# Performance work log

Measured on AMD Instinct MI355X. Metric: run time of the kernel, lower is better.

## Reference

```python
import jax, jax.numpy as jnp
import numpy as np

N, E = 100000, 1600000
D_IN, H, C = 128, 4, 32
NEG_SLOPE = 0.2

def setup_inputs() -> dict:
    key = jax.random.key(0)
    ks = jax.random.split(key, 6)
    x = jax.random.normal(ks[0], (N, D_IN), dtype=jnp.float32)
    edge_index = jax.random.randint(ks[1], (2, E), 0, N, dtype=jnp.int64)
    s = 1.0 / np.sqrt(D_IN)
    W_l = jax.random.normal(ks[2], (D_IN, H * C), dtype=jnp.float32) * s
    W_r = jax.random.normal(ks[3], (D_IN, H * C), dtype=jnp.float32) * s
    att = jax.random.normal(ks[4], (H, C), dtype=jnp.float32) * (1.0 / np.sqrt(C))
    bias = jax.random.normal(ks[5], (H * C,), dtype=jnp.float32) * 0.01
    return {"x": x, "edge_index": edge_index, "W_l": W_l, "W_r": W_r, "att": att, "bias": bias}

def reference(x, edge_index, W_l, W_r, att, bias):
    # GATv2: e_ij = att . LeakyReLU(W_l x_j + W_r x_i); softmax over incoming edges of i;
    # out_i = sum_j alpha_ij * (W_l x_j); heads concatenated, then bias.
    src, dst = edge_index[0], edge_index[1]
    n = x.shape[0]
    xl = (x @ W_l).reshape(n, H, C)   # source transform (lin_l)
    xr = (x @ W_r).reshape(n, H, C)   # target transform (lin_r)
    xj = xl[src]                       # [E,H,C] gathered source feats
    xi = xr[dst]                       # [E,H,C] gathered target feats
    e = jax.nn.leaky_relu(xi + xj, NEG_SLOPE)
    score = jnp.einsum('ehc,hc->eh', e, att)          # [E,H]
    # segment softmax over destination nodes
    m = jax.ops.segment_max(score, dst, num_segments=n)  # [N,H]
    ex = jnp.exp(score - m[dst])
    denom = jax.ops.segment_sum(ex, dst, num_segments=n)  # [N,H]
    alpha = ex / (denom[dst] + 1e-16)                      # [E,H]
    out = jax.ops.segment_sum(alpha[..., None] * xj, dst, num_segments=n)  # [N,H,C]
    return out.reshape(n, H * C) + bias
```

## Files before the change

### kernel.cpp

```cpp
#include <hip/hip_runtime.h>
#include <hip/hip_bf16.h>
#include <math.h>

#define N_NODES 100000
#define E_EDGES 1600000
#define D 128
#define NEG_SLOPE 0.2f

#define BSH   8
#define NBKT  391
#define BCAP  4992
#define P1_EPB 8192
#define P1_TPB 512
#define P1_EPT 16

typedef __bf16 bf16x8 __attribute__((ext_vector_type(8)));
typedef float f32x4 __attribute__((ext_vector_type(4)));
typedef float f32x2 __attribute__((ext_vector_type(2)));

__device__ __forceinline__ float bf2f(unsigned short u) {
    union { unsigned int i; float f; } x; x.i = ((unsigned int)u) << 16; return x.f;
}
__device__ __forceinline__ unsigned short f2bf(float f) {
    union { float f; unsigned int i; } x; x.f = f;
    unsigned int r = x.i + 0x7fffu + ((x.i >> 16) & 1u);
    return (unsigned short)(r >> 16);
}
__device__ __forceinline__ void unpack4p(uint2 u, f32x2* lo, f32x2* hi) {
    union { unsigned int i; float f; } a, b, c, d;
    a.i = u.x << 16; b.i = u.x & 0xffff0000u;
    c.i = u.y << 16; d.i = u.y & 0xffff0000u;
    *lo = (f32x2){a.f, b.f}; *hi = (f32x2){c.f, d.f};
}
__device__ __forceinline__ f32x2 pabs(f32x2 v) {
    union { f32x2 f; unsigned int u[2]; } x; x.f = v;
    x.u[0] &= 0x7fffffffu; x.u[1] &= 0x7fffffffu;
    return x.f;
}

__global__ void GATv2Conv_56908316672629_kernel(
    const unsigned int* ei_words, int* flags,
    const float* __restrict__ Wl, const float* __restrict__ Wr,
    unsigned short* __restrict__ wtg, int* __restrict__ bcur)
{
    __shared__ int cnt_edge;
    const int tid = threadIdx.x;
    const int bid = blockIdx.x;

    if (bid == 0) {
        for (int i = tid; i < NBKT; i += 256) bcur[i] = 0;
    }
    if (bid == 1) {
        if (tid == 0) cnt_edge = 0;
        __syncthreads();
        unsigned int w = ei_words[2 * tid + 1];
        if (w != 0u) atomicAdd(&cnt_edge, 1);
        __syncthreads();
        if (tid == 0) flags[0] = (cnt_edge == 0) ? 1 : 0;
    }

    const int gid = bid * 256 + tid;
    const int sel = gid >> 14;
    const int rem = gid & 16383;
    const int k = rem >> 7, n = rem & 127;
    const float* W = sel ? Wr : Wl;
    wtg[(size_t)sel * 16384 + n * 128 + k] = f2bf(W[k * 128 + n]);
}

__global__ __launch_bounds__(256) void gemm_f32_kernel(
    const float* __restrict__ X,
    const unsigned short* __restrict__ wtg,
    unsigned short* __restrict__ xl, unsigned short* __restrict__ xr)
{
    __shared__ unsigned short Xs[128][136];

    const int rowbase = blockIdx.x * 128;
    const int tid = threadIdx.x;

    for (int c = tid; c < 4096; c += 256) {
        int r = c >> 5, k4 = (c & 31) << 2;
        int grow = rowbase + r;
        float4 v = make_float4(0.f, 0.f, 0.f, 0.f);
        if (grow < N_NODES) v = ((const float4*)(X + (size_t)grow * D))[c & 31];
        union { unsigned short us[4]; uint2 u2; } pk;
        pk.us[0] = f2bf(v.x); pk.us[1] = f2bf(v.y);
        pk.us[2] = f2bf(v.z); pk.us[3] = f2bf(v.w);
        *((uint2*)&Xs[r][k4]) = pk.u2;
    }
    __syncthreads();

    const int wave = tid >> 6, lane = tid & 63;
    const int mrow = lane & 15, quad = lane >> 4;

    for (int sel = 0; sel < 2; ++sel) {
        const bf16x8* wt = (const bf16x8*)(wtg + (size_t)sel * 16384);
        unsigned short* out = sel ? xr : xl;

        f32x4 accA[8], accB[8];
#pragma unroll
        for (int i = 0; i < 8; ++i) {
            accA[i] = (f32x4){0.f, 0.f, 0.f, 0.f};
            accB[i] = (f32x4){0.f, 0.f, 0.f, 0.f};
        }

#pragma unroll
        for (int kk = 0; kk < 4; ++kk) {
            const int k0 = kk * 32 + quad * 8;
            bf16x8 afA = *(const bf16x8*)&Xs[wave * 16 + mrow][k0];
            bf16x8 afB = *(const bf16x8*)&Xs[64 + wave * 16 + mrow][k0];
            const bf16x8* wk = wt + mrow * 16 + kk * 4 + quad;
#pragma unroll
            for (int n0 = 0; n0 < 8; ++n0) {
                bf16x8 bfrag = wk[n0 * 256];
                accA[n0] = __builtin_amdgcn_mfma_f32_16x16x32_bf16(afA, bfrag, accA[n0], 0, 0, 0);
                accB[n0] = __builtin_amdgcn_mfma_f32_16x16x32_bf16(afB, bfrag, accB[n0], 0, 0, 0);
            }
        }

        const int growA = rowbase + wave * 16 + quad * 4;
        const int growB = growA + 64;
#pragma unroll
        for (int n0 = 0; n0 < 8; ++n0) {
            int col = n0 * 16 + mrow;
#pragma unroll
            for (int r = 0; r < 4; ++r) {
                int ga = growA + r, gb2 = growB + r;
                if (ga < N_NODES) out[(size_t)ga * D + col] = f2bf(accA[n0][r]);
                if (gb2 < N_NODES) out[(size_t)gb2 * D + col] = f2bf(accB[n0][r]);
            }
        }
    }
}

__device__ __forceinline__ unsigned int edge_word(const unsigned int* ei, int is64,
                                                  long long entry) {
    return is64 ? ei[2 * entry] : ei[entry];
}

__global__ __launch_bounds__(P1_TPB) void bucket_scatter_kernel(
    const unsigned int* __restrict__ ei, const int* __restrict__ flags,
    int* __restrict__ bcur, unsigned int* __restrict__ pairbuf)
{
    __shared__ int h[NBKT];
    __shared__ int gbase[NBKT];

    const int tid = threadIdx.x;
    const int is64 = flags[0];
    const long long e0 = (long long)blockIdx.x * P1_EPB;

    unsigned int sv[P1_EPT], dv[P1_EPT];
#pragma unroll
    for (int j = 0; j < P1_EPT; ++j) {
        long long e = e0 + j * P1_TPB + tid;
        unsigned int s = 0u, d = 0xffffffffu;
        if (e < E_EDGES) {
            s = edge_word(ei, is64, e);
            d = edge_word(ei, is64, (long long)E_EDGES + e);
            if (s >= N_NODES || d >= N_NODES) d = 0xffffffffu;
        }
        sv[j] = s; dv[j] = d;
    }

    for (int i = tid; i < NBKT; i += P1_TPB) h[i] = 0;
    __syncthreads();

#pragma unroll
    for (int j = 0; j < P1_EPT; ++j)
        if (dv[j] != 0xffffffffu) atomicAdd(&h[dv[j] >> BSH], 1);
    __syncthreads();

    for (int i = tid; i < NBKT; i += P1_TPB) {
        int c = h[i];
        gbase[i] = c ? atomicAdd(&bcur[i], c) : 0;
        h[i] = 0;
    }
    __syncthreads();

#pragma unroll
    for (int j = 0; j < P1_EPT; ++j) {
        unsigned int d = dv[j];
        if (d != 0xffffffffu) {
            int b = (int)(d >> BSH);
            int r = gbase[b] + atomicAdd(&h[b], 1);
            if (r < BCAP)
                pairbuf[(size_t)b * BCAP + r] = sv[j] | ((d & 255u) << 24);
        }
    }
}

__global__ __launch_bounds__(256) void bucket_sort_kernel(
    const int* __restrict__ bcur, unsigned int* __restrict__ pairbuf,
    int* __restrict__ rowstart, int* __restrict__ rowend)
{
    __shared__ unsigned int stage[BCAP];
    __shared__ int cnt[256];
    __shared__ int base[256];

    const int b = blockIdx.x;
    const int tid = threadIdx.x;
    int n = bcur[b]; if (n > BCAP) n = BCAP;
    unsigned int* buf = pairbuf + (size_t)b * BCAP;

    for (int i = tid; i < n; i += 256) stage[i] = buf[i];
    cnt[tid] = 0;
    __syncthreads();

    for (int i = tid; i < n; i += 256) atomicAdd(&cnt[stage[i] >> 24], 1);
    __syncthreads();

    int v = cnt[tid];
    base[tid] = v;
    __syncthreads();
    for (int off = 1; off < 256; off <<= 1) {
        int u = (tid >= off) ? base[tid - off] : 0;
        __syncthreads();
        base[tid] += u;
        __syncthreads();
    }
    const int myend = base[tid];
    const int mystart = myend - v;

    const int node = b * 256 + tid;
    if (node < N_NODES) {
        rowstart[node] = b * BCAP + mystart;
        rowend[node]   = b * BCAP + myend;
    }

    cnt[tid] = mystart;
    __syncthreads();

    for (int i = tid; i < n; i += 256) {
        unsigned int p = stage[i];
        int pos = atomicAdd(&cnt[p >> 24], 1);
        buf[pos] = p & 0x00FFFFFFu;
    }
}

__global__ __launch_bounds__(256) void aggregate_kernel(
    const unsigned short* __restrict__ xl, const unsigned short* __restrict__ xr,
    const int* __restrict__ rowstart, const int* __restrict__ rowend,
    const int* __restrict__ ssrc,
    const float* __restrict__ att, const float* __restrict__ bias,
    float* __restrict__ out)
{
    const int t = threadIdx.x & 31;
    const int node = blockIdx.x * 8 + (threadIdx.x >> 5);
    if (node >= N_NODES) return;
    const int f0 = t * 4;

    f32x2 xr0, xr1;
    unpack4p(*(const uint2*)&xr[(size_t)node * D + f0], &xr0, &xr1);
    const float4 av = *(const float4*)&att[f0];
    f32x2 a60 = (f32x2){0.6f * av.x, 0.6f * av.y};
    f32x2 a61 = (f32x2){0.6f * av.z, 0.6f * av.w};
    f32x2 a40 = (f32x2){0.4f * av.x, 0.4f * av.y};
    f32x2 a41 = (f32x2){0.4f * av.z, 0.4f * av.w};

    const uint2* xlp = (const uint2*)xl + (f0 >> 2);

    const int p0 = rowstart[node];
    const int p1 = rowend[node];

    float l = 0.f;
    f32x2 acc0 = (f32x2){0.f, 0.f}, acc1 = (f32x2){0.f, 0.f};

#define ESCORE(u, xa0, xa1, pe)                                   \
    {                                                             \
        unpack4p(u, &xa0, &xa1);                                  \
        f32x2 v0 = xa0 + xr0, v1 = xa1 + xr1;                     \
        f32x2 pp = v0 * a60;                                      \
        pp += pabs(v0) * a40;                                     \
        pp += v1 * a61;                                           \
        pp += pabs(v1) * a41;                                     \
        pe = pp.x + pp.y;                                         \
    }

    int p = p0;
    for (; p + 8 <= p1; p += 8) {
        int s0 = ssrc[p],     s1 = ssrc[p + 1], s2 = ssrc[p + 2], s3 = ssrc[p + 3];
        int s4 = ssrc[p + 4], s5 = ssrc[p + 5], s6 = ssrc[p + 6], s7 = ssrc[p + 7];
        uint2 u0 = xlp[(size_t)s0 * 32];
        uint2 u1 = xlp[(size_t)s1 * 32];
        uint2 u2 = xlp[(size_t)s2 * 32];
        uint2 u3 = xlp[(size_t)s3 * 32];
        uint2 u4 = xlp[(size_t)s4 * 32];
        uint2 u5 = xlp[(size_t)s5 * 32];
        uint2 u6 = xlp[(size_t)s6 * 32];
        uint2 u7 = xlp[(size_t)s7 * 32];
        f32x2 xa0, xa1, xb0, xb1, xc0, xc1, xd0, xd1;
        f32x2 xe0, xe1, xf0, xf1, xg0, xg1, xh0, xh1;
        float e0, e1, e2, e3, e4, e5, e6, e7;
        ESCORE(u0, xa0, xa1, e0);
        ESCORE(u1, xb0, xb1, e1);
        ESCORE(u2, xc0, xc1, e2);
        ESCORE(u3, xd0, xd1, e3);
        ESCORE(u4, xe0, xe1, e4);
        ESCORE(u5, xf0, xf1, e5);
        ESCORE(u6, xg0, xg1, e6);
        ESCORE(u7, xh0, xh1, e7);
#pragma unroll
        for (int off = 1; off < 8; off <<= 1) {
            e0 += __shfl_xor(e0, off);
            e1 += __shfl_xor(e1, off);
            e2 += __shfl_xor(e2, off);
            e3 += __shfl_xor(e3, off);
            e4 += __shfl_xor(e4, off);
            e5 += __shfl_xor(e5, off);
            e6 += __shfl_xor(e6, off);
            e7 += __shfl_xor(e7, off);
        }
        float w0 = __expf(e0), w1 = __expf(e1), w2 = __expf(e2), w3 = __expf(e3);
        float w4 = __expf(e4), w5 = __expf(e5), w6 = __expf(e6), w7 = __expf(e7);
        l += ((w0 + w1) + (w2 + w3)) + ((w4 + w5) + (w6 + w7));
        acc0 += w0 * xa0; acc1 += w0 * xa1;
        acc0 += w1 * xb0; acc1 += w1 * xb1;
        acc0 += w2 * xc0; acc1 += w2 * xc1;
        acc0 += w3 * xd0; acc1 += w3 * xd1;
        acc0 += w4 * xe0; acc1 += w4 * xe1;
        acc0 += w5 * xf0; acc1 += w5 * xf1;
        acc0 += w6 * xg0; acc1 += w6 * xg1;
        acc0 += w7 * xh0; acc1 += w7 * xh1;
    }
    for (; p + 4 <= p1; p += 4) {
        int s0 = ssrc[p], s1 = ssrc[p + 1], s2 = ssrc[p + 2], s3 = ssrc[p + 3];
        uint2 u0 = xlp[(size_t)s0 * 32];
        uint2 u1 = xlp[(size_t)s1 * 32];
        uint2 u2 = xlp[(size_t)s2 * 32];
        uint2 u3 = xlp[(size_t)s3 * 32];
        f32x2 xa0, xa1, xb0, xb1, xc0, xc1, xd0, xd1;
        float e0, e1, e2, e3;
        ESCORE(u0, xa0, xa1, e0);
        ESCORE(u1, xb0, xb1, e1);
        ESCORE(u2, xc0, xc1, e2);
        ESCORE(u3, xd0, xd1, e3);
#pragma unroll
        for (int off = 1; off < 8; off <<= 1) {
            e0 += __shfl_xor(e0, off);
            e1 += __shfl_xor(e1, off);
            e2 += __shfl_xor(e2, off);
            e3 += __shfl_xor(e3, off);
        }
        float w0 = __expf(e0), w1 = __expf(e1), w2 = __expf(e2), w3 = __expf(e3);
        l += (w0 + w1) + (w2 + w3);
        acc0 += w0 * xa0; acc1 += w0 * xa1;
        acc0 += w1 * xb0; acc1 += w1 * xb1;
        acc0 += w2 * xc0; acc1 += w2 * xc1;
        acc0 += w3 * xd0; acc1 += w3 * xd1;
    }
    for (; p < p1; ++p) {
        int s0 = ssrc[p];
        uint2 u0 = xlp[(size_t)s0 * 32];
        f32x2 xa0, xa1;
        float e0;
        ESCORE(u0, xa0, xa1, e0);
#pragma unroll
        for (int off = 1; off < 8; off <<= 1) e0 += __shfl_xor(e0, off);
        float w0 = __expf(e0);
        l += w0;
        acc0 += w0 * xa0; acc1 += w0 * xa1;
    }
#undef ESCORE

    const float inv = (l > 0.f) ? (1.f / l) : 0.f;
    const float4 bv = *(const float4*)&bias[f0];
    float4 o;
    o.x = fmaf(acc0.x, inv, bv.x);
    o.y = fmaf(acc0.y, inv, bv.y);
    o.z = fmaf(acc1.x, inv, bv.z);
    o.w = fmaf(acc1.y, inv, bv.w);
    *(float4*)&out[(size_t)node * D + f0] = o;
}

extern "C" void kernel_launch(void* const* d_in, const int* in_sizes, int n_in,
                              void* d_out, int out_size, void* d_ws, size_t ws_size,
                              hipStream_t stream)
{
    const float*        X    = (const float*)d_in[0];
    const unsigned int* ei   = (const unsigned int*)d_in[1];
    const float*        Wl   = (const float*)d_in[2];
    const float*        Wr   = (const float*)d_in[3];
    const float*        att  = (const float*)d_in[4];
    const float*        bias = (const float*)d_in[5];

    char* ws = (char*)d_ws;
    size_t off = 0;
    unsigned short* xl = (unsigned short*)(ws + off); off += (size_t)N_NODES * D * 2;
    unsigned short* xr = (unsigned short*)(ws + off); off += (size_t)N_NODES * D * 2;
    unsigned int* pairbuf = (unsigned int*)(ws + off); off += (size_t)NBKT * BCAP * 4;
    int* rowstart = (int*)(ws + off); off += (size_t)N_NODES * 4;
    int* rowend   = (int*)(ws + off); off += (size_t)N_NODES * 4;
    int* bcur     = (int*)(ws + off); off += (size_t)((NBKT + 255) & ~255) * 4;
    int* flags    = (int*)(ws + off); off += 256;
    unsigned short* wtg = (unsigned short*)(ws + off); off += 2 * 128 * 128 * 2;

    const int gb = (N_NODES + 127) / 128;
    const int p1b = (E_EDGES + P1_EPB - 1) / P1_EPB;

    GATv2Conv_56908316672629_kernel<<<128, 256, 0, stream>>>(ei, flags, Wl, Wr, wtg, bcur);

    gemm_f32_kernel<<<gb, 256, 0, stream>>>(X, wtg, xl, xr);

    bucket_scatter_kernel<<<p1b, P1_TPB, 0, stream>>>(ei, flags, bcur, pairbuf);
    bucket_sort_kernel<<<NBKT, 256, 0, stream>>>(bcur, pairbuf, rowstart, rowend);

    aggregate_kernel<<<(N_NODES + 7) / 8, 256, 0, stream>>>(
        xl, xr, rowstart, rowend, (const int*)pairbuf, att, bias, (float*)d_out);
}
```

Measured before the change: 283.5 us.

## Group nodes by in-degree within each bucket to balance aggregate warps

The bucket sort kernel now counting-sorts the 256 nodes of each bucket by in-degree, capped at 63, and writes a permutation array. The aggregate kernel reads that permutation so each block handles nodes of similar degree, which is meant to reduce warp divergence and load imbalance. It also removes the 8-edge unrolled loop and keeps only the 4-edge loop. The cost is an extra indirection, extra blocks covering padded node slots, and less memory-level parallelism per iteration.

```diff
diff --git a/kernel.cpp b/kernel.cpp
--- a/kernel.cpp
+++ b/kernel.cpp
@@ -190,11 +190,14 @@
 
 __global__ __launch_bounds__(256) void bucket_sort_kernel(
     const int* __restrict__ bcur, unsigned int* __restrict__ pairbuf,
-    int* __restrict__ rowstart, int* __restrict__ rowend)
+    int* __restrict__ rowstart, int* __restrict__ rowend,
+    int* __restrict__ order)
 {
     __shared__ unsigned int stage[BCAP];
     __shared__ int cnt[256];
     __shared__ int base[256];
+    __shared__ int dh[64];
+    __shared__ int dcur[64];
 
     const int b = blockIdx.x;
     const int tid = threadIdx.x;
@@ -203,12 +206,15 @@
 
     for (int i = tid; i < n; i += 256) stage[i] = buf[i];
     cnt[tid] = 0;
+    if (tid < 64) dh[tid] = 0;
     __syncthreads();
 
     for (int i = tid; i < n; i += 256) atomicAdd(&cnt[stage[i] >> 24], 1);
     __syncthreads();
 
     int v = cnt[tid];
+    const int bin = (v < 63) ? v : 63;
+    atomicAdd(&dh[bin], 1);
     base[tid] = v;
     __syncthreads();
     for (int off = 1; off < 256; off <<= 1) {
@@ -220,6 +226,21 @@
     const int myend = base[tid];
     const int mystart = myend - v;
 
+    if (tid < 64) {
+        int x = dh[tid];
+        int inc = x;
+#pragma unroll
+        for (int off = 1; off < 64; off <<= 1) {
+            int u = __shfl_up(inc, off);
+            if (tid >= off) inc += u;
+        }
+        dcur[tid] = inc - x;
+    }
+    __syncthreads();
+
+    const int rank = atomicAdd(&dcur[bin], 1);
+    order[b * 256 + rank] = b * 256 + tid;
+
     const int node = b * 256 + tid;
     if (node < N_NODES) {
         rowstart[node] = b * BCAP + mystart;
@@ -239,12 +260,13 @@
 __global__ __launch_bounds__(256) void aggregate_kernel(
     const unsigned short* __restrict__ xl, const unsigned short* __restrict__ xr,
     const int* __restrict__ rowstart, const int* __restrict__ rowend,
-    const int* __restrict__ ssrc,
+    const int* __restrict__ ssrc, const int* __restrict__ order,
     const float* __restrict__ att, const float* __restrict__ bias,
     float* __restrict__ out)
 {
     const int t = threadIdx.x & 31;
-    const int node = blockIdx.x * 8 + (threadIdx.x >> 5);
+    const int g = blockIdx.x * 8 + (threadIdx.x >> 5);
+    const int node = order[g];
     if (node >= N_NODES) return;
     const int f0 = t * 4;
 
@@ -276,51 +298,6 @@
     }
 
     int p = p0;
-    for (; p + 8 <= p1; p += 8) {
-        int s0 = ssrc[p],     s1 = ssrc[p + 1], s2 = ssrc[p + 2], s3 = ssrc[p + 3];
-        int s4 = ssrc[p + 4], s5 = ssrc[p + 5], s6 = ssrc[p + 6], s7 = ssrc[p + 7];
-        uint2 u0 = xlp[(size_t)s0 * 32];
-        uint2 u1 = xlp[(size_t)s1 * 32];
-        uint2 u2 = xlp[(size_t)s2 * 32];
-        uint2 u3 = xlp[(size_t)s3 * 32];
-        uint2 u4 = xlp[(size_t)s4 * 32];
-        uint2 u5 = xlp[(size_t)s5 * 32];
-        uint2 u6 = xlp[(size_t)s6 * 32];
-        uint2 u7 = xlp[(size_t)s7 * 32];
-        f32x2 xa0, xa1, xb0, xb1, xc0, xc1, xd0, xd1;
-        f32x2 xe0, xe1, xf0, xf1, xg0, xg1, xh0, xh1;
-        float e0, e1, e2, e3, e4, e5, e6, e7;
-        ESCORE(u0, xa0, xa1, e0);
-        ESCORE(u1, xb0, xb1, e1);
-        ESCORE(u2, xc0, xc1, e2);
-        ESCORE(u3, xd0, xd1, e3);
-        ESCORE(u4, xe0, xe1, e4);
-        ESCORE(u5, xf0, xf1, e5);
-        ESCORE(u6, xg0, xg1, e6);
-        ESCORE(u7, xh0, xh1, e7);
-#pragma unroll
-        for (int off = 1; off < 8; off <<= 1) {
-            e0 += __shfl_xor(e0, off);
-            e1 += __shfl_xor(e1, off);
-            e2 += __shfl_xor(e2, off);
-            e3 += __shfl_xor(e3, off);
-            e4 += __shfl_xor(e4, off);
-            e5 += __shfl_xor(e5, off);
-            e6 += __shfl_xor(e6, off);
-            e7 += __shfl_xor(e7, off);
-        }
-        float w0 = __expf(e0), w1 = __expf(e1), w2 = __expf(e2), w3 = __expf(e3);
-        float w4 = __expf(e4), w5 = __expf(e5), w6 = __expf(e6), w7 = __expf(e7);
-        l += ((w0 + w1) + (w2 + w3)) + ((w4 + w5) + (w6 + w7));
-        acc0 += w0 * xa0; acc1 += w0 * xa1;
-        acc0 += w1 * xb0; acc1 += w1 * xb1;
-        acc0 += w2 * xc0; acc1 += w2 * xc1;
-        acc0 += w3 * xd0; acc1 += w3 * xd1;
-        acc0 += w4 * xe0; acc1 += w4 * xe1;
-        acc0 += w5 * xf0; acc1 += w5 * xf1;
-        acc0 += w6 * xg0; acc1 += w6 * xg1;
-        acc0 += w7 * xh0; acc1 += w7 * xh1;
-    }
     for (; p + 4 <= p1; p += 4) {
         int s0 = ssrc[p], s1 = ssrc[p + 1], s2 = ssrc[p + 2], s3 = ssrc[p + 3];
         uint2 u0 = xlp[(size_t)s0 * 32];
@@ -389,6 +366,7 @@
     unsigned int* pairbuf = (unsigned int*)(ws + off); off += (size_t)NBKT * BCAP * 4;
     int* rowstart = (int*)(ws + off); off += (size_t)N_NODES * 4;
     int* rowend   = (int*)(ws + off); off += (size_t)N_NODES * 4;
+    int* order    = (int*)(ws + off); off += (size_t)NBKT * 256 * 4;
     int* bcur     = (int*)(ws + off); off += (size_t)((NBKT + 255) & ~255) * 4;
     int* flags    = (int*)(ws + off); off += 256;
     unsigned short* wtg = (unsigned short*)(ws + off); off += 2 * 128 * 128 * 2;
@@ -401,8 +379,8 @@
     gemm_f32_kernel<<<gb, 256, 0, stream>>>(X, wtg, xl, xr);
 
     bucket_scatter_kernel<<<p1b, P1_TPB, 0, stream>>>(ei, flags, bcur, pairbuf);
-    bucket_sort_kernel<<<NBKT, 256, 0, stream>>>(bcur, pairbuf, rowstart, rowend);
-
-    aggregate_kernel<<<(N_NODES + 7) / 8, 256, 0, stream>>>(
-        xl, xr, rowstart, rowend, (const int*)pairbuf, att, bias, (float*)d_out);
-}
+    bucket_sort_kernel<<<NBKT, 256, 0, stream>>>(bcur, pairbuf, rowstart, rowend, order);
+
+    aggregate_kernel<<<(NBKT * 256) / 8, 256, 0, stream>>>(
+        xl, xr, rowstart, rowend, (const int*)pairbuf, order, att, bias, (float*)d_out);
+}
```

Result: faster. 277.6 us (-2.1%).
